# Optimization experiments

Hardware: AMD Instinct MI355X
Metric: run time of the kernel (lower is better)

Reference implementation:

```python
import jax, jax.numpy as jnp
import numpy as np

NUM_EXPERTS = 64
TOP_K = 8
LOAD_EMA_DECAY = 0.999
BIAS_TEMPERATURE = 1.0
NOISE_STD = 0.01


def setup_inputs() -> dict:
    key = jax.random.key(0)
    k1, k2, k3, k4 = jax.random.split(key, 4)
    hidden_states = jax.random.normal(k1, (4, 4096, 2048), dtype=jnp.float32)
    router_w = jax.random.normal(k2, (NUM_EXPERTS, 2048), dtype=jnp.float32) * 0.02
    expert_loads = jax.random.uniform(k3, (NUM_EXPERTS,), dtype=jnp.float32)
    bias_strength = jnp.ones((1,), dtype=jnp.float32)
    noise = jax.random.normal(k4, (4 * 4096, NUM_EXPERTS), dtype=jnp.float32)
    return {
        "hidden_states": hidden_states,
        "router_w": router_w,
        "expert_loads": expert_loads,
        "bias_strength": bias_strength,
        "noise": noise,
    }


def reference(hidden_states, router_w, expert_loads, bias_strength, noise):
    # Training-mode forward with total_routed > 0 (adaptive bias active),
    # balance_loss_weight = 0 (aux_loss is None in the original).
    E = NUM_EXPERTS
    x = hidden_states.reshape(-1, hidden_states.shape[-1])  # [N, d]
    n_tokens = x.shape[0]

    # Router linear (no bias) + training noise
    logits = jnp.einsum("nd,ed->ne", x, router_w) + noise * NOISE_STD  # [N, E]

    # Adaptive load-based bias (core of aux-loss-free routing)
    q = expert_loads / jnp.clip(expert_loads.sum(), 1e-8)  # normalized loads
    t = 1.0 / E  # expected uniform load
    # F.kl_div(log q, t, reduction='sum') = sum_e t*(log t - log q_e)
    kl = jnp.sum(t * (jnp.log(t) - jnp.log(jnp.clip(q, 1e-8))))
    adaptive_strength = jax.nn.sigmoid(kl * 10.0)
    new_bias_strength = 0.9 * bias_strength[0] + 0.1 * adaptive_strength
    bias = jnp.tanh((q - t) * E) * BIAS_TEMPERATURE * new_bias_strength  # [E]
    logits = logits - bias[None, :]

    # Top-k selection + softmax gating over selected logits
    expert_weights, expert_indices = jax.lax.top_k(logits, TOP_K)  # [N, K]
    expert_weights = jax.nn.softmax(expert_weights, axis=-1)

    # EMA load-statistics update (scatter-add of gate weights per expert)
    batch_loads = jax.ops.segment_sum(
        expert_weights.reshape(-1), expert_indices.reshape(-1), num_segments=E
    ) / n_tokens
    new_expert_loads = LOAD_EMA_DECAY * expert_loads + (1.0 - LOAD_EMA_DECAY) * batch_loads

    return expert_indices, expert_weights, new_expert_loads, new_bias_strength
```

## Files before the change

kernel.cpp:

```cpp
#include <hip/hip_runtime.h>
#include <hip/hip_bf16.h>
#include <math.h>

#define NT 16384
#define DIM 2048
#define NE 64
#define TK 8

typedef _Float16 f16_t;
typedef _Float16 half8 __attribute__((ext_vector_type(8)));
typedef float floatx16 __attribute__((ext_vector_type(16)));

typedef __attribute__((address_space(3))) unsigned int  lds_u32;
typedef __attribute__((address_space(1))) const unsigned int gbl_u32;

__global__ __launch_bounds__(256) void prep_kernel(const float* __restrict__ w,
                                                   const float* __restrict__ expert_loads,
                                                   const float* __restrict__ bias_strength,
                                                   float* __restrict__ ws_bias,
                                                   float* __restrict__ ws_batch,
                                                   f16_t* __restrict__ whi,
                                                   f16_t* __restrict__ wlo,
                                                   float* __restrict__ out_bias_strength) {
    if (blockIdx.x == 64) {
        int e = threadIdx.x;
        if (e < 64) {
            float load = expert_loads[e];
            float s = load;
            #pragma unroll
            for (int off = 32; off >= 1; off >>= 1) s += __shfl_xor(s, off, 64);
            s = fmaxf(s, 1e-8f);
            float q = load / s;
            const float t = 1.0f / 64.0f;
            float kl = t * (logf(t) - logf(fmaxf(q, 1e-8f)));
            #pragma unroll
            for (int off = 32; off >= 1; off >>= 1) kl += __shfl_xor(kl, off, 64);
            float as = 1.0f / (1.0f + expf(-10.0f * kl));
            float nbs = 0.9f * bias_strength[0] + 0.1f * as;
            ws_bias[e] = tanhf((q - t) * 64.0f) * nbs;
            ws_batch[e] = 0.0f;
            if (e == 0) out_bias_strength[0] = nbs;
        }
        return;
    }
    int idx = blockIdx.x * 256 + threadIdx.x;
    int lane = idx & 63;
    int tile = (idx >> 6) & 1;
    int c    = idx >> 7;
    int n = tile * 32 + (lane & 31);
    int k = c * 16 + (lane >> 5) * 8;
    const float* src = w + (size_t)n * DIM + k;
    float4 a = *(const float4*)src;
    float4 b = *(const float4*)(src + 4);
    float v[8] = {a.x, a.y, a.z, a.w, b.x, b.y, b.z, b.w};
    half8 h, l;
    #pragma unroll
    for (int j = 0; j < 8; ++j) {
        f16_t hh = (f16_t)v[j];
        h[j] = hh;
        l[j] = (f16_t)(v[j] - (float)hh);
    }
    *(half8*)(whi + (size_t)idx * 8) = h;
    *(half8*)(wlo + (size_t)idx * 8) = l;
}

__global__ __launch_bounds__(512, 4) void router_main(const float* __restrict__ x,
                                                      const f16_t* __restrict__ whi,
                                                      const f16_t* __restrict__ wlo,
                                                      const float* __restrict__ noise,
                                                      const float* __restrict__ ws_bias,
                                                      float* __restrict__ ws_batch,
                                                      float* __restrict__ out) {
    __shared__ float smem[17408];
    __shared__ float bias_sh[64];
    __shared__ float loads_sh[64];

    const int tid = threadIdx.x;
    const int wv  = tid >> 6;
    const int L   = tid & 63;
    const int r   = L & 31;
    const int kh  = L >> 5;
    const int token0 = blockIdx.x * 32;

    if (tid < 64) { bias_sh[tid] = ws_bias[tid]; loads_sh[tid] = 0.0f; }

    char* mybuf = (char*)smem + wv * 8320;
    const half8* whi8 = (const half8*)whi;
    const half8* wlo8 = (const half8*)wlo;

    floatx16 acc0, acc1;
    #pragma unroll
    for (int i = 0; i < 16; ++i) { acc0[i] = 0.0f; acc1[i] = 0.0f; }

    const int srow = L >> 4;
    const int sb   = (L & 15) * 16;
    const float* xbase = x + (size_t)token0 * DIM + wv * 256;

    const int gfrag = r >> 2;
    const int mfrag = r & 3;

    for (int ch = 0; ch < 4; ++ch) {
        asm volatile("s_waitcnt lgkmcnt(0)" ::: "memory");
        #pragma unroll
        for (int g = 0; g < 8; ++g) {
            const char* gp = (const char*)(xbase + (size_t)(4 * g + srow) * DIM + ch * 64) + sb;
            __builtin_amdgcn_global_load_lds((gbl_u32*)gp, (lds_u32*)(mybuf + g * 1040), 16, 0, 0);
        }
        asm volatile("s_waitcnt vmcnt(0)" ::: "memory");

        #pragma unroll
        for (int cc = 0; cc < 4; ++cc) {
            const int c16 = wv * 16 + ch * 4 + cc;
            const float* fp = (const float*)(mybuf + gfrag * 1040 + mfrag * 256 + cc * 64 + kh * 32);
            float4 a0 = *(const float4*)fp;
            float4 a1 = *(const float4*)(fp + 4);
            float xv[8] = {a0.x, a0.y, a0.z, a0.w, a1.x, a1.y, a1.z, a1.w};
            half8 ah, al;
            #pragma unroll
            for (int j = 0; j < 8; ++j) {
                f16_t h = (f16_t)xv[j];
                ah[j] = h;
                al[j] = (f16_t)(xv[j] - (float)h);
            }
            const int bidx = (c16 * 2) * 64 + L;
            half8 b0h = whi8[bidx];
            half8 b1h = whi8[bidx + 64];
            half8 b0l = wlo8[bidx];
            half8 b1l = wlo8[bidx + 64];
            acc0 = __builtin_amdgcn_mfma_f32_32x32x16_f16(ah, b0h, acc0, 0, 0, 0);
            acc1 = __builtin_amdgcn_mfma_f32_32x32x16_f16(ah, b1h, acc1, 0, 0, 0);
            acc0 = __builtin_amdgcn_mfma_f32_32x32x16_f16(al, b0h, acc0, 0, 0, 0);
            acc1 = __builtin_amdgcn_mfma_f32_32x32x16_f16(al, b1h, acc1, 0, 0, 0);
            acc0 = __builtin_amdgcn_mfma_f32_32x32x16_f16(ah, b0l, acc0, 0, 0, 0);
            acc1 = __builtin_amdgcn_mfma_f32_32x32x16_f16(ah, b1l, acc1, 0, 0, 0);
        }
    }

    __syncthreads();

    #pragma unroll
    for (int reg = 0; reg < 16; ++reg) {
        int row = (reg & 3) + 8 * (reg >> 2) + 4 * kh;
        smem[wv * 2176 + row * 68 + r]      = acc0[reg];
        smem[wv * 2176 + row * 68 + 32 + r] = acc1[reg];
    }
    __syncthreads();

    #pragma unroll
    for (int p = 0; p < 4; ++p) {
        int o = tid + p * 512;
        int t = o >> 6, e = o & 63;
        float s = 0.0f;
        #pragma unroll
        for (int q = 0; q < 8; ++q) s += smem[q * 2176 + t * 68 + e];
        s += noise[(size_t)(token0 + t) * NE + e] * 0.01f - bias_sh[e];
        smem[t * 68 + e] = s;
    }
    __syncthreads();

    if (tid < 32) {
        int t = tid;
        float tv[TK]; int ti_[TK];
        #pragma unroll
        for (int j = 0; j < TK; ++j) { tv[j] = -INFINITY; ti_[j] = 0; }
        for (int e = 0; e < NE; ++e) {
            float v = smem[t * 68 + e]; int id = e;
            #pragma unroll
            for (int j = 0; j < TK; ++j) {
                bool gt = v > tv[j];
                float nv = gt ? v : tv[j];
                int   ni = gt ? id : ti_[j];
                float ov = gt ? tv[j] : v;
                int   oi = gt ? ti_[j] : id;
                tv[j] = nv; ti_[j] = ni; v = ov; id = oi;
            }
        }
        float m = tv[0], ssum = 0.0f, wvv[TK];
        #pragma unroll
        for (int j = 0; j < TK; ++j) { wvv[j] = expf(tv[j] - m); ssum += wvv[j]; }
        float inv = 1.0f / ssum;
        size_t gt_ = (size_t)(token0 + t);
        #pragma unroll
        for (int j = 0; j < TK; ++j) {
            float wgt = wvv[j] * inv;
            out[gt_ * TK + j] = (float)ti_[j];
            out[(size_t)NT * TK + gt_ * TK + j] = wgt;
            atomicAdd(&loads_sh[ti_[j]], wgt);
        }
    }
    __syncthreads();
    if (tid < 64) atomicAdd(&ws_batch[tid], loads_sh[tid]);
}

__global__ __launch_bounds__(64) void finalize_kernel(const float* __restrict__ expert_loads,
                                                      const float* __restrict__ ws_batch,
                                                      float* __restrict__ out_loads) {
    int e = threadIdx.x;
    out_loads[e] = 0.999f * expert_loads[e] + 0.001f * (ws_batch[e] / (float)NT);
}

extern "C" void kernel_launch(void* const* d_in, const int* in_sizes, int n_in,
                              void* d_out, int out_size, void* d_ws, size_t ws_size,
                              hipStream_t stream) {
    const float* x     = (const float*)d_in[0];
    const float* rw    = (const float*)d_in[1];
    const float* loads = (const float*)d_in[2];
    const float* bs    = (const float*)d_in[3];
    const float* noise = (const float*)d_in[4];
    float* out = (float*)d_out;
    float* ws  = (float*)d_ws;
    float* ws_bias  = ws;
    float* ws_batch = ws + 64;
    f16_t* whi = (f16_t*)(ws + 128);
    f16_t* wlo = whi + (size_t)16384 * 8;

    prep_kernel<<<65, 256, 0, stream>>>(rw, loads, bs, ws_bias, ws_batch, whi, wlo,
                                        out + (size_t)NT * TK * 2 + NE);
    router_main<<<NT / 32, 512, 0, stream>>>(x, whi, wlo, noise, ws_bias, ws_batch, out);
    finalize_kernel<<<1, 64, 0, stream>>>(loads, ws_batch, out + (size_t)NT * TK * 2);
}
```

Measured before the change: 221.4 us.

## Convert x tiles to packed fp16 hi/lo once in LDS, shared across waves

Replaces the per-wave asynchronous global-to-LDS loads of raw fp32 x with cooperative register loads. Each x element is split into fp16 hi/lo once and stored packed in a shared LDS tile, and the eight waves then read it back for their own K slices. This removes redundant fp32-to-fp16 split work and halves LDS bytes per element, but adds two block-wide barriers per stage and loses the direct-to-LDS asynchronous load path. The K loop now runs over eight 256-column stages.

```diff
diff --git a/kernel.cpp b/kernel.cpp
--- a/kernel.cpp
+++ b/kernel.cpp
@@ -11,8 +11,7 @@
 typedef _Float16 half8 __attribute__((ext_vector_type(8)));
 typedef float floatx16 __attribute__((ext_vector_type(16)));
 
-typedef __attribute__((address_space(3))) unsigned int  lds_u32;
-typedef __attribute__((address_space(1))) const unsigned int gbl_u32;
+union H8U4 { uint4 u; half8 h; };
 
 __global__ __launch_bounds__(256) void prep_kernel(const float* __restrict__ w,
                                                    const float* __restrict__ expert_loads,
@@ -84,7 +83,7 @@
 
     if (tid < 64) { bias_sh[tid] = ws_bias[tid]; loads_sh[tid] = 0.0f; }
 
-    char* mybuf = (char*)smem + wv * 8320;
+    unsigned int* xt = (unsigned int*)smem;
     const half8* whi8 = (const half8*)whi;
     const half8* wlo8 = (const half8*)wlo;
 
@@ -92,47 +91,56 @@
     #pragma unroll
     for (int i = 0; i < 16; ++i) { acc0[i] = 0.0f; acc1[i] = 0.0f; }
 
-    const int srow = L >> 4;
-    const int sb   = (L & 15) * 16;
-    const float* xbase = x + (size_t)token0 * DIM + wv * 256;
-
-    const int gfrag = r >> 2;
-    const int mfrag = r & 3;
-
-    for (int ch = 0; ch < 4; ++ch) {
-        asm volatile("s_waitcnt lgkmcnt(0)" ::: "memory");
-        #pragma unroll
-        for (int g = 0; g < 8; ++g) {
-            const char* gp = (const char*)(xbase + (size_t)(4 * g + srow) * DIM + ch * 64) + sb;
-            __builtin_amdgcn_global_load_lds((gbl_u32*)gp, (lds_u32*)(mybuf + g * 1040), 16, 0, 0);
-        }
-        asm volatile("s_waitcnt vmcnt(0)" ::: "memory");
-
-        #pragma unroll
-        for (int cc = 0; cc < 4; ++cc) {
-            const int c16 = wv * 16 + ch * 4 + cc;
-            const float* fp = (const float*)(mybuf + gfrag * 1040 + mfrag * 256 + cc * 64 + kh * 32);
-            float4 a0 = *(const float4*)fp;
-            float4 a1 = *(const float4*)(fp + 4);
-            float xv[8] = {a0.x, a0.y, a0.z, a0.w, a1.x, a1.y, a1.z, a1.w};
-            half8 ah, al;
-            #pragma unroll
-            for (int j = 0; j < 8; ++j) {
-                f16_t h = (f16_t)xv[j];
-                ah[j] = h;
-                al[j] = (f16_t)(xv[j] - (float)h);
+    for (int s = 0; s < 8; ++s) {
+        __syncthreads();
+        #pragma unroll
+        for (int q = 0; q < 4; ++q) {
+            const int row = wv + q * 8;
+            float4 v4 = *(const float4*)(x + (size_t)(token0 + row) * DIM + s * 256 + L * 4);
+            uint4 p;
+            {
+                f16_t h0 = (f16_t)v4.x, h1 = (f16_t)v4.y, h2 = (f16_t)v4.z, h3 = (f16_t)v4.w;
+                f16_t l0 = (f16_t)(v4.x - (float)h0), l1 = (f16_t)(v4.y - (float)h1);
+                f16_t l2 = (f16_t)(v4.z - (float)h2), l3 = (f16_t)(v4.w - (float)h3);
+                p.x = (unsigned int)__builtin_bit_cast(unsigned short, h0) |
+                      ((unsigned int)__builtin_bit_cast(unsigned short, l0) << 16);
+                p.y = (unsigned int)__builtin_bit_cast(unsigned short, h1) |
+                      ((unsigned int)__builtin_bit_cast(unsigned short, l1) << 16);
+                p.z = (unsigned int)__builtin_bit_cast(unsigned short, h2) |
+                      ((unsigned int)__builtin_bit_cast(unsigned short, l2) << 16);
+                p.w = (unsigned int)__builtin_bit_cast(unsigned short, h3) |
+                      ((unsigned int)__builtin_bit_cast(unsigned short, l3) << 16);
             }
+            *(uint4*)(xt + row * 260 + L * 4) = p;
+        }
+        __syncthreads();
+        #pragma unroll
+        for (int cc = 0; cc < 2; ++cc) {
+            const int jw  = wv * 2 + cc;
+            const int c16 = s * 16 + jw;
+            const unsigned int* fp = xt + r * 260 + jw * 16 + kh * 8;
+            uint4 u0 = *(const uint4*)fp;
+            uint4 u1 = *(const uint4*)(fp + 4);
+            H8U4 ah, al;
+            ah.u.x = (u0.x & 0xFFFFu) | (u0.y << 16);
+            ah.u.y = (u0.z & 0xFFFFu) | (u0.w << 16);
+            ah.u.z = (u1.x & 0xFFFFu) | (u1.y << 16);
+            ah.u.w = (u1.z & 0xFFFFu) | (u1.w << 16);
+            al.u.x = (u0.x >> 16) | (u0.y & 0xFFFF0000u);
+            al.u.y = (u0.z >> 16) | (u0.w & 0xFFFF0000u);
+            al.u.z = (u1.x >> 16) | (u1.y & 0xFFFF0000u);
+            al.u.w = (u1.z >> 16) | (u1.w & 0xFFFF0000u);
             const int bidx = (c16 * 2) * 64 + L;
             half8 b0h = whi8[bidx];
             half8 b1h = whi8[bidx + 64];
             half8 b0l = wlo8[bidx];
             half8 b1l = wlo8[bidx + 64];
-            acc0 = __builtin_amdgcn_mfma_f32_32x32x16_f16(ah, b0h, acc0, 0, 0, 0);
-            acc1 = __builtin_amdgcn_mfma_f32_32x32x16_f16(ah, b1h, acc1, 0, 0, 0);
-            acc0 = __builtin_amdgcn_mfma_f32_32x32x16_f16(al, b0h, acc0, 0, 0, 0);
-            acc1 = __builtin_amdgcn_mfma_f32_32x32x16_f16(al, b1h, acc1, 0, 0, 0);
-            acc0 = __builtin_amdgcn_mfma_f32_32x32x16_f16(ah, b0l, acc0, 0, 0, 0);
-            acc1 = __builtin_amdgcn_mfma_f32_32x32x16_f16(ah, b1l, acc1, 0, 0, 0);
+            acc0 = __builtin_amdgcn_mfma_f32_32x32x16_f16(ah.h, b0h, acc0, 0, 0, 0);
+            acc1 = __builtin_amdgcn_mfma_f32_32x32x16_f16(ah.h, b1h, acc1, 0, 0, 0);
+            acc0 = __builtin_amdgcn_mfma_f32_32x32x16_f16(al.h, b0h, acc0, 0, 0, 0);
+            acc1 = __builtin_amdgcn_mfma_f32_32x32x16_f16(al.h, b1h, acc1, 0, 0, 0);
+            acc0 = __builtin_amdgcn_mfma_f32_32x32x16_f16(ah.h, b0l, acc0, 0, 0, 0);
+            acc1 = __builtin_amdgcn_mfma_f32_32x32x16_f16(ah.h, b1l, acc1, 0, 0, 0);
         }
     }
 
@@ -150,11 +158,11 @@
     for (int p = 0; p < 4; ++p) {
         int o = tid + p * 512;
         int t = o >> 6, e = o & 63;
-        float s = 0.0f;
-        #pragma unroll
-        for (int q = 0; q < 8; ++q) s += smem[q * 2176 + t * 68 + e];
-        s += noise[(size_t)(token0 + t) * NE + e] * 0.01f - bias_sh[e];
-        smem[t * 68 + e] = s;
+        float sum = 0.0f;
+        #pragma unroll
+        for (int q = 0; q < 8; ++q) sum += smem[q * 2176 + t * 68 + e];
+        sum += noise[(size_t)(token0 + t) * NE + e] * 0.01f - bias_sh[e];
+        smem[t * 68 + e] = sum;
     }
     __syncthreads();
 
```

After: 218.7 us. No clear change (-1.2%).
